# Kernel optimization log

Hardware: AMD Instinct MI355X
Metric: run time of the kernel (lower is better)

## Reference

```python
import jax, jax.numpy as jnp
import numpy as np
import math

DIM = 2048
NUM_HEADS = 16
NUM_KV_HEADS = 4
HEAD_DIM = DIM // NUM_HEADS  # 128
KV_DIM = DIM * NUM_KV_HEADS // NUM_HEADS  # 512
B, T = 4, 2048


def setup_inputs() -> dict:
    key = jax.random.key(0)
    ks = jax.random.split(key, 12)
    s = 0.02
    return {
        "x": jax.random.normal(ks[0], (B, T, DIM), dtype=jnp.float32),
        "cos": jax.random.uniform(ks[1], (T, HEAD_DIM // 2), dtype=jnp.float32),
        "sin": jax.random.uniform(ks[2], (T, HEAD_DIM // 2), dtype=jnp.float32),
        "Wq": jax.random.normal(ks[3], (DIM, DIM), dtype=jnp.float32) * s,
        "bq": jnp.zeros((DIM,), dtype=jnp.float32),
        "Wk": jax.random.normal(ks[4], (DIM, KV_DIM), dtype=jnp.float32) * s,
        "bk": jnp.zeros((KV_DIM,), dtype=jnp.float32),
        "Wv": jax.random.normal(ks[5], (DIM, KV_DIM), dtype=jnp.float32) * s,
        "bv": jnp.zeros((KV_DIM,), dtype=jnp.float32),
        "Wo": jax.random.normal(ks[6], (DIM, DIM), dtype=jnp.float32) * s,
        "bo": jnp.zeros((DIM,), dtype=jnp.float32),
    }


def _rope(t, cos, sin):
    # t: [B, H, T, D]; cos/sin: [T, D/2] broadcast over (B, H)
    t1, t2 = t[..., ::2], t[..., 1::2]
    return jnp.concatenate([t1 * cos - t2 * sin, t1 * sin + t2 * cos], axis=-1)


def reference(x, cos, sin, Wq, bq, Wk, bk, Wv, bv, Wo, bo):
    Bx, Tx, C = x.shape
    q = (x @ Wq + bq).reshape(Bx, Tx, NUM_HEADS, HEAD_DIM).transpose(0, 2, 1, 3)
    k = (x @ Wk + bk).reshape(Bx, Tx, NUM_KV_HEADS, HEAD_DIM).transpose(0, 2, 1, 3)
    v = (x @ Wv + bv).reshape(Bx, Tx, NUM_KV_HEADS, HEAD_DIM).transpose(0, 2, 1, 3)
    rep = NUM_HEADS // NUM_KV_HEADS
    k = jnp.repeat(k, rep, axis=1)
    v = jnp.repeat(v, rep, axis=1)
    q = _rope(q, cos, sin)
    k = _rope(k, cos, sin)
    scores = jnp.einsum("bhqd,bhkd->bhqk", q, k) / math.sqrt(HEAD_DIM)
    attn = jax.nn.softmax(scores, axis=-1)
    out = jnp.einsum("bhqk,bhkd->bhqd", attn, v)
    out = out.transpose(0, 2, 1, 3).reshape(Bx, Tx, C)
    return out @ Wo + bo
```

## Files before the change

### kernel.cpp

```cpp
#include <hip/hip_runtime.h>

typedef unsigned short u16;
using bf16x8 = __attribute__((ext_vector_type(8))) short;
using u16x8  = __attribute__((ext_vector_type(8))) unsigned short;
using f32x4  = __attribute__((ext_vector_type(4))) float;
using u32x2  = __attribute__((ext_vector_type(2))) unsigned int;

__device__ __forceinline__ u16 f2bf(float f) {
  unsigned u = __float_as_uint(f);
  u += 0x7FFFu + ((u >> 16) & 1u);
  return (u16)(u >> 16);
}

__device__ __forceinline__ unsigned cvt_pk_bf16(float lo, float hi) {
  unsigned r;
  asm("v_cvt_pk_bf16_f32 %0, %1, %2" : "=v"(r) : "v"(lo), "v"(hi));
  return r;
}

__device__ __forceinline__ void gload_lds16(const void* g, void* l) {
  __builtin_amdgcn_global_load_lds(
      (const __attribute__((address_space(1))) unsigned int*)g,
      (__attribute__((address_space(3))) unsigned int*)l, 16, 0, 0);
}

__global__ __launch_bounds__(256) void k_cvt(const float* __restrict__ src,
                                             u16* __restrict__ dst) {
  size_t i = (size_t)blockIdx.x * 256 + threadIdx.x;
  const float4* s4 = (const float4*)src;
  float4 a = s4[i * 2], b = s4[i * 2 + 1];
  u16x8 r;
  r[0] = f2bf(a.x); r[1] = f2bf(a.y); r[2] = f2bf(a.z); r[3] = f2bf(a.w);
  r[4] = f2bf(b.x); r[5] = f2bf(b.y); r[6] = f2bf(b.z); r[7] = f2bf(b.w);
  *(u16x8*)(dst + i * 8) = r;
}

__global__ void k_transpose_cvt(const float* __restrict__ src, u16* __restrict__ dst,
                                int R, int C) {
  __shared__ float tile[32][33];
  int bx = blockIdx.x * 32, by = blockIdx.y * 32;
  int tx = threadIdx.x, ty = threadIdx.y;
#pragma unroll
  for (int j = 0; j < 4; ++j)
    tile[ty + j * 8][tx] = src[(size_t)(by + ty + j * 8) * C + bx + tx];
  __syncthreads();
#pragma unroll
  for (int j = 0; j < 4; ++j)
    dst[(size_t)(bx + ty + j * 8) * R + by + tx] = f2bf(tile[tx][ty + j * 8]);
}

template <int EPI>
__global__ __launch_bounds__(512, 2) void k_gemm256(
    const u16* __restrict__ A, const u16* __restrict__ Bt,
    const float* __restrict__ bq, const float* __restrict__ bk, const float* __restrict__ bv,
    const float* __restrict__ cosb, const float* __restrict__ sinb,
    u16* __restrict__ qbuf, u16* __restrict__ kbuf, u16* __restrict__ vbufT,
    const float* __restrict__ bo, float* __restrict__ fout, int ntiles) {
  __shared__ u16 As[2][2][128 * 64];
  __shared__ u16 Bs[2][2][128 * 64];

  const int nwg = 32 * ntiles;
  const int per = nwg >> 3;
  const int sid = ((int)blockIdx.x & 7) * per + ((int)blockIdx.x >> 3);
  const int mt = sid & 31;
  const int nt = sid >> 5;

  const int tid = threadIdx.x, lane = tid & 63, w = tid >> 6;
  const int lm = lane & 15, lg = lane >> 4;
  const int wr = w >> 2, wc = w & 3;

  const u16* Abase = A  + (size_t)mt * 256 * 2048;
  const u16* Bbase = Bt + (size_t)nt * 256 * 2048;

  f32x4 acc[8][4];
#pragma unroll
  for (int mf = 0; mf < 8; ++mf)
#pragma unroll
    for (int nf = 0; nf < 4; ++nf) { f32x4 z = {0.f, 0.f, 0.f, 0.f}; acc[mf][nf] = z; }

  auto stage = [&](int d, int kt) {
#pragma unroll
    for (int j = 0; j < 2; ++j) {
      const int s = w * 2 + j;
      const int c = s * 64 + lane;
      const int row = c >> 3;
      const int col = ((c & 7) ^ (row & 7)) << 3;
#pragma unroll
      for (int h = 0; h < 2; ++h) {
        gload_lds16(Abase + (size_t)(h * 128 + row) * 2048 + kt + col, &As[d][h][s * 512]);
        gload_lds16(Bbase + (size_t)(h * 128 + row) * 2048 + kt + col, &Bs[d][h][s * 512]);
      }
    }
  };

  stage(0, 0);
  for (int t = 0; t < 32; ++t) {
    if (t < 31) {
      stage((t + 1) & 1, (t + 1) << 6);
      asm volatile("s_waitcnt vmcnt(8)" ::: "memory");
    } else {
      asm volatile("s_waitcnt vmcnt(0)" ::: "memory");
    }
    __builtin_amdgcn_s_barrier();
    __builtin_amdgcn_sched_barrier(0);

    const int d = t & 1;
    const u16* Ah = &As[d][wr][0];
    const u16* Bh = &Bs[d][wc >> 1][0];
    const int brow0 = (wc & 1) * 64;

    bf16x8 bfr[4][2];
#pragma unroll
    for (int nf = 0; nf < 4; ++nf)
#pragma unroll
      for (int k2 = 0; k2 < 2; ++k2) {
        const int row = brow0 + nf * 16 + lm;
        bfr[nf][k2] = *(const bf16x8*)(Bh + row * 64 + ((((k2 << 2) + lg) ^ (lm & 7)) << 3));
      }
#pragma unroll
    for (int mp = 0; mp < 4; ++mp) {
      bf16x8 af[2][2];
#pragma unroll
      for (int mi = 0; mi < 2; ++mi)
#pragma unroll
        for (int k2 = 0; k2 < 2; ++k2) {
          const int row = (mp * 2 + mi) * 16 + lm;
          af[mi][k2] = *(const bf16x8*)(Ah + row * 64 + ((((k2 << 2) + lg) ^ (lm & 7)) << 3));
        }
      __builtin_amdgcn_s_setprio(1);
#pragma unroll
      for (int mi = 0; mi < 2; ++mi)
#pragma unroll
        for (int k2 = 0; k2 < 2; ++k2)
#pragma unroll
          for (int nf = 0; nf < 4; ++nf)
            acc[mp * 2 + mi][nf] = __builtin_amdgcn_mfma_f32_16x16x32_bf16(
                af[mi][k2], bfr[nf][k2], acc[mp * 2 + mi][nf], 0, 0, 0);
      __builtin_amdgcn_s_setprio(0);
    }
    __builtin_amdgcn_sched_barrier(0);
    __builtin_amdgcn_s_barrier();
  }

  const int row0 = mt * 256 + wr * 128 + lg * 4;
  const int col0 = nt * 256 + wc * 64 + lm;
  const float qscale = 0.12751744f;

#pragma unroll
  for (int mf = 0; mf < 8; ++mf) {
#pragma unroll
    for (int nf = 0; nf < 4; ++nf) {
      const int gc = col0 + nf * 16;
#pragma unroll
      for (int i = 0; i < 4; ++i) {
        const int gr = row0 + mf * 16 + i;
        float v = acc[mf][nf][i];
        if (EPI == 1) {
          fout[(size_t)gr * 2048 + gc] = v + bo[gc];
        } else {
          const int b = gr >> 11, tt = gr & 2047;
          if (nt < 8) {
            const int h = gc >> 7, dd0 = gc & 127;
            float val = v + bq[gc];
            float part = __shfl_xor(val, 1);
            const int ir = dd0 >> 1;
            float c = cosb[tt * 64 + ir], s = sinb[tt * 64 + ir];
            float outv; int dd;
            if (dd0 & 1) { outv = part * s + val * c; dd = ir + 64; }
            else         { outv = val * c - part * s; dd = ir; }
            qbuf[(((size_t)(b * 16 + h) * 2048 + tt) << 7) + dd] = f2bf(outv * qscale);
          } else if (nt < 10) {
            const int g2 = gc - 2048;
            const int kvh = g2 >> 7, dd0 = g2 & 127;
            float val = v + bk[g2];
            float part = __shfl_xor(val, 1);
            const int ir = dd0 >> 1;
            float c = cosb[tt * 64 + ir], s = sinb[tt * 64 + ir];
            float outv; int dd;
            if (dd0 & 1) { outv = part * s + val * c; dd = ir + 64; }
            else         { outv = val * c - part * s; dd = ir; }
            kbuf[(((size_t)(b * 4 + kvh) * 2048 + tt) << 7) + dd] = f2bf(outv);
          } else {
            const int g2 = gc - 2560;
            const int kvh = g2 >> 7, dd0 = g2 & 127;
            float val = v + bv[g2];
            vbufT[((size_t)((b * 4 + kvh) * 128 + dd0)) * 2048 + tt] = f2bf(val);
          }
        }
      }
    }
  }
}

__global__ __launch_bounds__(256, 2) void k_attn(const u16* __restrict__ qbuf,
                                                 const u16* __restrict__ kbuf,
                                                 const u16* __restrict__ vbufT,
                                                 u16* __restrict__ ob) {
  __shared__ u16 Ks[2][64 * 128];
  __shared__ u16 Vs[2][128 * 64];
  __shared__ u16 Ps[128 * 64];

  const int f = blockIdx.x;
  const int x = f & 7, mm = f >> 3;
  const int g = x * 2 + (mm >> 6);
  const int mem = mm & 63;
  const int b = g >> 2, kvh = g & 3;
  const int h = kvh * 4 + (mem >> 4);
  const int qt = mem & 15;

  const int tid = threadIdx.x, lane = tid & 63, w = tid >> 6;
  const int lm = lane & 15, lg = lane >> 4;

  const u16* qb = qbuf + ((size_t)((b * 16 + h) * 2048 + qt * 128)) * 128;
  const u16* kb = kbuf + ((size_t)(b * 4 + kvh) * 2048) * 128;
  const u16* vb = vbufT + ((size_t)(b * 4 + kvh) * 128) * 2048;

  bf16x8 qf[2][4];
#pragma unroll
  for (int st = 0; st < 2; ++st)
#pragma unroll
    for (int dc = 0; dc < 4; ++dc)
      qf[st][dc] = *(const bf16x8*)(qb + (size_t)(w * 32 + st * 16 + lm) * 128 + dc * 32 + (lg << 3));

  f32x4 o[2][8];
#pragma unroll
  for (int st = 0; st < 2; ++st)
#pragma unroll
    for (int dn = 0; dn < 8; ++dn) { f32x4 z = {0.f, 0.f, 0.f, 0.f}; o[st][dn] = z; }
  float lsum[2] = {0.f, 0.f};

  auto stage = [&](int buf, int kt) {
#pragma unroll
    for (int j = 0; j < 4; ++j) {
      int s  = w * 4 + j;
      int cK = s * 64 + lane;
      int rK = cK >> 4, ccK = cK & 15;
      gload_lds16(kb + (size_t)(kt + rK) * 128 + ((ccK ^ (rK & 7)) << 3), &Ks[buf][s << 9]);
      int dV = s * 8 + (lane >> 3), ccV = lane & 7;
      gload_lds16(vb + (size_t)dV * 2048 + kt + ((ccV ^ (dV & 7)) << 3), &Vs[buf][s << 9]);
    }
  };

  stage(0, 0);
  int cur = 0;
  for (int t = 0; t < 32; ++t) {
    const int kt = t << 6;
    if (t < 31) {
      stage(cur ^ 1, kt + 64);
      asm volatile("s_waitcnt vmcnt(8)" ::: "memory");
    } else {
      asm volatile("s_waitcnt vmcnt(0)" ::: "memory");
    }
    __builtin_amdgcn_s_barrier();
    __builtin_amdgcn_sched_barrier(0);
    const u16* KsC = Ks[cur];
    const u16* VsC = Vs[cur];

#pragma unroll
    for (int kg = 0; kg < 4; ++kg) {
      const int krow = kg * 16 + lm;
      bf16x8 kf[4];
#pragma unroll
      for (int dc = 0; dc < 4; ++dc)
        kf[dc] = *(const bf16x8*)(KsC + krow * 128 + (((dc * 4 + lg) ^ (krow & 7)) << 3));
      f32x4 s0 = {0.f, 0.f, 0.f, 0.f}, s1 = {0.f, 0.f, 0.f, 0.f};
      __builtin_amdgcn_s_setprio(1);
#pragma unroll
      for (int dc = 0; dc < 4; ++dc) {
        s0 = __builtin_amdgcn_mfma_f32_16x16x32_bf16(kf[dc], qf[0][dc], s0, 0, 0, 0);
        s1 = __builtin_amdgcn_mfma_f32_16x16x32_bf16(kf[dc], qf[1][dc], s1, 0, 0, 0);
      }
      __builtin_amdgcn_s_setprio(0);
#pragma unroll
      for (int st = 0; st < 2; ++st) {
        f32x4 sv = st ? s1 : s0;
        float p0 = __builtin_amdgcn_exp2f(sv[0]);
        float p1 = __builtin_amdgcn_exp2f(sv[1]);
        float p2 = __builtin_amdgcn_exp2f(sv[2]);
        float p3 = __builtin_amdgcn_exp2f(sv[3]);
        lsum[st] += (p0 + p1) + (p2 + p3);
        u32x2 pk;
        pk[0] = cvt_pk_bf16(p0, p1);
        pk[1] = cvt_pk_bf16(p2, p3);
        const int q = w * 32 + st * 16 + lm;
        const int chunk = kg * 2 + (lg >> 1);
        u16* dst = Ps + q * 64 + ((chunk ^ (q & 7)) << 3) + ((lg & 1) << 2);
        *reinterpret_cast<u32x2*>(dst) = pk;
      }
    }

#pragma unroll
    for (int kstep = 0; kstep < 2; ++kstep) {
      bf16x8 pf[2];
#pragma unroll
      for (int st = 0; st < 2; ++st) {
        const int q = w * 32 + st * 16 + lm;
        pf[st] = *(const bf16x8*)(Ps + q * 64 + (((kstep * 4 + lg) ^ (q & 7)) << 3));
      }
      __builtin_amdgcn_s_setprio(1);
#pragma unroll
      for (int dn = 0; dn < 8; ++dn) {
        const int d = dn * 16 + lm;
        bf16x8 vf = *(const bf16x8*)(VsC + d * 64 + (((kstep * 4 + lg) ^ (d & 7)) << 3));
        o[0][dn] = __builtin_amdgcn_mfma_f32_16x16x32_bf16(pf[0], vf, o[0][dn], 0, 0, 0);
        o[1][dn] = __builtin_amdgcn_mfma_f32_16x16x32_bf16(pf[1], vf, o[1][dn], 0, 0, 0);
      }
      __builtin_amdgcn_s_setprio(0);
    }
    __builtin_amdgcn_sched_barrier(0);
    __builtin_amdgcn_s_barrier();
    cur ^= 1;
  }

#pragma unroll
  for (int st = 0; st < 2; ++st) {
    float L = lsum[st];
    L += __shfl_xor(L, 16);
    L += __shfl_xor(L, 32);
#pragma unroll
    for (int i = 0; i < 4; ++i) {
      float inv = 1.0f / __shfl(L, lg * 4 + i);
      int t = qt * 128 + w * 32 + st * 16 + lg * 4 + i;
#pragma unroll
      for (int dn = 0; dn < 8; ++dn) {
        int d = dn * 16 + lm;
        ob[((size_t)(b * 2048 + t)) * 2048 + h * 128 + d] = f2bf(o[st][dn][i] * inv);
      }
    }
  }
}

extern "C" void kernel_launch(void* const* d_in, const int* in_sizes, int n_in,
                              void* d_out, int out_size, void* d_ws, size_t ws_size,
                              hipStream_t stream) {
  const float* x    = (const float*)d_in[0];
  const float* cosb = (const float*)d_in[1];
  const float* sinb = (const float*)d_in[2];
  const float* Wq   = (const float*)d_in[3];
  const float* bq   = (const float*)d_in[4];
  const float* Wk   = (const float*)d_in[5];
  const float* bk   = (const float*)d_in[6];
  const float* Wv   = (const float*)d_in[7];
  const float* bv   = (const float*)d_in[8];
  const float* Wo   = (const float*)d_in[9];
  const float* bo   = (const float*)d_in[10];
  float* out = (float*)d_out;

  u16* ws    = (u16*)d_ws;
  u16* xb    = ws;
  u16* wqkvT = xb    + (size_t)8192 * 2048;
  u16* woT   = wqkvT + (size_t)3072 * 2048;
  u16* qbuf  = woT   + (size_t)2048 * 2048;
  u16* kbuf  = qbuf  + (size_t)8192 * 2048;
  u16* vbufT = kbuf  + (size_t)8192 * 512;
  u16* attn  = xb;

  k_cvt<<<8192, 256, 0, stream>>>(x, xb);
  dim3 tb(32, 8);
  k_transpose_cvt<<<dim3(64, 64), tb, 0, stream>>>(Wq, wqkvT, 2048, 2048);
  k_transpose_cvt<<<dim3(16, 64), tb, 0, stream>>>(Wk, wqkvT + (size_t)2048 * 2048, 2048, 512);
  k_transpose_cvt<<<dim3(16, 64), tb, 0, stream>>>(Wv, wqkvT + (size_t)2560 * 2048, 2048, 512);
  k_transpose_cvt<<<dim3(64, 64), tb, 0, stream>>>(Wo, woT, 2048, 2048);

  k_gemm256<0><<<384, 512, 0, stream>>>(xb, wqkvT, bq, bk, bv, cosb, sinb,
                                        qbuf, kbuf, vbufT, nullptr, nullptr, 12);
  k_attn<<<1024, 256, 0, stream>>>(qbuf, kbuf, vbufT, attn);
  k_gemm256<1><<<256, 512, 0, stream>>>(attn, woT, nullptr, nullptr, nullptr, nullptr, nullptr,
                                        nullptr, nullptr, nullptr, bo, out, 8);
}
```

Before: 444.1 us.

## Shrink GEMM tiles to 256x128 with BK=32 for higher occupancy

Both projection GEMMs move from 256x256 tiles with K-step 64 to 256x128 tiles with K-step 32. This cuts shared memory and accumulator registers per workgroup, so launch bounds can ask for 4 workgroups per CU and the grid doubles to 768 and 512 workgroups. The LDS swizzle and the wait counts are reworked to match. In exchange there are twice as many barrier-synchronised K iterations, and each workgroup does fewer MFMAs between loads, so data reuse drops.

```diff
diff --git a/kernel.cpp b/kernel.cpp
--- a/kernel.cpp
+++ b/kernel.cpp
@@ -50,16 +50,16 @@
 }
 
 template <int EPI>
-__global__ __launch_bounds__(512, 2) void k_gemm256(
+__global__ __launch_bounds__(512, 4) void k_gemm(
     const u16* __restrict__ A, const u16* __restrict__ Bt,
     const float* __restrict__ bq, const float* __restrict__ bk, const float* __restrict__ bv,
     const float* __restrict__ cosb, const float* __restrict__ sinb,
     u16* __restrict__ qbuf, u16* __restrict__ kbuf, u16* __restrict__ vbufT,
-    const float* __restrict__ bo, float* __restrict__ fout, int ntiles) {
-  __shared__ u16 As[2][2][128 * 64];
-  __shared__ u16 Bs[2][2][128 * 64];
-
-  const int nwg = 32 * ntiles;
+    const float* __restrict__ bo, float* __restrict__ fout, int ntn) {
+  __shared__ u16 As[2][256 * 32];
+  __shared__ u16 Bs[2][128 * 32];
+
+  const int nwg = 32 * ntn;
   const int per = nwg >> 3;
   const int sid = ((int)blockIdx.x & 7) * per + ((int)blockIdx.x >> 3);
   const int mt = sid & 31;
@@ -67,37 +67,37 @@
 
   const int tid = threadIdx.x, lane = tid & 63, w = tid >> 6;
   const int lm = lane & 15, lg = lane >> 4;
-  const int wr = w >> 2, wc = w & 3;
+  const int wr = w >> 1, wc = w & 1;
+  const int sw = (lm >> 1) & 3;
 
   const u16* Abase = A  + (size_t)mt * 256 * 2048;
-  const u16* Bbase = Bt + (size_t)nt * 256 * 2048;
-
-  f32x4 acc[8][4];
-#pragma unroll
-  for (int mf = 0; mf < 8; ++mf)
+  const u16* Bbase = Bt + (size_t)nt * 128 * 2048;
+
+  f32x4 acc[4][4];
+#pragma unroll
+  for (int mf = 0; mf < 4; ++mf)
 #pragma unroll
     for (int nf = 0; nf < 4; ++nf) { f32x4 z = {0.f, 0.f, 0.f, 0.f}; acc[mf][nf] = z; }
 
   auto stage = [&](int d, int kt) {
 #pragma unroll
     for (int j = 0; j < 2; ++j) {
-      const int s = w * 2 + j;
-      const int c = s * 64 + lane;
-      const int row = c >> 3;
-      const int col = ((c & 7) ^ (row & 7)) << 3;
-#pragma unroll
-      for (int h = 0; h < 2; ++h) {
-        gload_lds16(Abase + (size_t)(h * 128 + row) * 2048 + kt + col, &As[d][h][s * 512]);
-        gload_lds16(Bbase + (size_t)(h * 128 + row) * 2048 + kt + col, &Bs[d][h][s * 512]);
-      }
-    }
+      const int c = (w * 2 + j) * 64 + lane;
+      const int row = c >> 2;
+      const int cc = (c & 3) ^ ((row >> 1) & 3);
+      gload_lds16(Abase + (size_t)row * 2048 + kt + cc * 8, &As[d][(w * 2 + j) * 512]);
+    }
+    const int c = w * 64 + lane;
+    const int row = c >> 2;
+    const int cc = (c & 3) ^ ((row >> 1) & 3);
+    gload_lds16(Bbase + (size_t)row * 2048 + kt + cc * 8, &Bs[d][w * 512]);
   };
 
   stage(0, 0);
-  for (int t = 0; t < 32; ++t) {
-    if (t < 31) {
-      stage((t + 1) & 1, (t + 1) << 6);
-      asm volatile("s_waitcnt vmcnt(8)" ::: "memory");
+  for (int t = 0; t < 64; ++t) {
+    if (t < 63) {
+      stage((t + 1) & 1, (t + 1) << 5);
+      asm volatile("s_waitcnt vmcnt(3)" ::: "memory");
     } else {
       asm volatile("s_waitcnt vmcnt(0)" ::: "memory");
     }
@@ -105,49 +105,34 @@
     __builtin_amdgcn_sched_barrier(0);
 
     const int d = t & 1;
-    const u16* Ah = &As[d][wr][0];
-    const u16* Bh = &Bs[d][wc >> 1][0];
-    const int brow0 = (wc & 1) * 64;
-
-    bf16x8 bfr[4][2];
-#pragma unroll
-    for (int nf = 0; nf < 4; ++nf)
-#pragma unroll
-      for (int k2 = 0; k2 < 2; ++k2) {
-        const int row = brow0 + nf * 16 + lm;
-        bfr[nf][k2] = *(const bf16x8*)(Bh + row * 64 + ((((k2 << 2) + lg) ^ (lm & 7)) << 3));
-      }
-#pragma unroll
-    for (int mp = 0; mp < 4; ++mp) {
-      bf16x8 af[2][2];
-#pragma unroll
-      for (int mi = 0; mi < 2; ++mi)
-#pragma unroll
-        for (int k2 = 0; k2 < 2; ++k2) {
-          const int row = (mp * 2 + mi) * 16 + lm;
-          af[mi][k2] = *(const bf16x8*)(Ah + row * 64 + ((((k2 << 2) + lg) ^ (lm & 7)) << 3));
-        }
-      __builtin_amdgcn_s_setprio(1);
-#pragma unroll
-      for (int mi = 0; mi < 2; ++mi)
-#pragma unroll
-        for (int k2 = 0; k2 < 2; ++k2)
-#pragma unroll
-          for (int nf = 0; nf < 4; ++nf)
-            acc[mp * 2 + mi][nf] = __builtin_amdgcn_mfma_f32_16x16x32_bf16(
-                af[mi][k2], bfr[nf][k2], acc[mp * 2 + mi][nf], 0, 0, 0);
-      __builtin_amdgcn_s_setprio(0);
-    }
+    bf16x8 bfr[4], af[4];
+#pragma unroll
+    for (int nf = 0; nf < 4; ++nf) {
+      const int row = wc * 64 + nf * 16 + lm;
+      bfr[nf] = *(const bf16x8*)(&Bs[d][row * 32 + ((lg ^ sw) << 3)]);
+    }
+#pragma unroll
+    for (int mf = 0; mf < 4; ++mf) {
+      const int row = wr * 64 + mf * 16 + lm;
+      af[mf] = *(const bf16x8*)(&As[d][row * 32 + ((lg ^ sw) << 3)]);
+    }
+    __builtin_amdgcn_s_setprio(1);
+#pragma unroll
+    for (int mf = 0; mf < 4; ++mf)
+#pragma unroll
+      for (int nf = 0; nf < 4; ++nf)
+        acc[mf][nf] = __builtin_amdgcn_mfma_f32_16x16x32_bf16(af[mf], bfr[nf], acc[mf][nf], 0, 0, 0);
+    __builtin_amdgcn_s_setprio(0);
     __builtin_amdgcn_sched_barrier(0);
     __builtin_amdgcn_s_barrier();
   }
 
-  const int row0 = mt * 256 + wr * 128 + lg * 4;
-  const int col0 = nt * 256 + wc * 64 + lm;
+  const int row0 = mt * 256 + wr * 64 + lg * 4;
+  const int col0 = nt * 128 + wc * 64 + lm;
   const float qscale = 0.12751744f;
 
 #pragma unroll
-  for (int mf = 0; mf < 8; ++mf) {
+  for (int mf = 0; mf < 4; ++mf) {
 #pragma unroll
     for (int nf = 0; nf < 4; ++nf) {
       const int gc = col0 + nf * 16;
@@ -159,7 +144,7 @@
           fout[(size_t)gr * 2048 + gc] = v + bo[gc];
         } else {
           const int b = gr >> 11, tt = gr & 2047;
-          if (nt < 8) {
+          if (nt < 16) {
             const int h = gc >> 7, dd0 = gc & 127;
             float val = v + bq[gc];
             float part = __shfl_xor(val, 1);
@@ -169,7 +154,7 @@
             if (dd0 & 1) { outv = part * s + val * c; dd = ir + 64; }
             else         { outv = val * c - part * s; dd = ir; }
             qbuf[(((size_t)(b * 16 + h) * 2048 + tt) << 7) + dd] = f2bf(outv * qscale);
-          } else if (nt < 10) {
+          } else if (nt < 20) {
             const int g2 = gc - 2048;
             const int kvh = g2 >> 7, dd0 = g2 & 127;
             float val = v + bk[g2];
@@ -362,9 +347,9 @@
   k_transpose_cvt<<<dim3(16, 64), tb, 0, stream>>>(Wv, wqkvT + (size_t)2560 * 2048, 2048, 512);
   k_transpose_cvt<<<dim3(64, 64), tb, 0, stream>>>(Wo, woT, 2048, 2048);
 
-  k_gemm256<0><<<384, 512, 0, stream>>>(xb, wqkvT, bq, bk, bv, cosb, sinb,
-                                        qbuf, kbuf, vbufT, nullptr, nullptr, 12);
+  k_gemm<0><<<768, 512, 0, stream>>>(xb, wqkvT, bq, bk, bv, cosb, sinb,
+                                     qbuf, kbuf, vbufT, nullptr, nullptr, 24);
   k_attn<<<1024, 256, 0, stream>>>(qbuf, kbuf, vbufT, attn);
-  k_gemm256<1><<<256, 512, 0, stream>>>(attn, woT, nullptr, nullptr, nullptr, nullptr, nullptr,
-                                        nullptr, nullptr, nullptr, bo, out, 8);
-}
+  k_gemm<1><<<512, 512, 0, stream>>>(attn, woT, nullptr, nullptr, nullptr, nullptr, nullptr,
+                                     nullptr, nullptr, nullptr, bo, out, 16);
+}
```

After: 421.9 us. 5.0% less time.

## Restructure GEMM main loop into four-phase ping-pong with interleaved LDS reads

Applied to the files above, without the earlier changes.

Rewrites the 256x256 bf16 GEMM K-loop into four MFMA sub-phases (quadrants of the wave tile). LDS fragment loads for the next quadrant sit between them, and the next K-tile's global-to-LDS prefetch is issued early in the iteration. Barriers and setprio around each phase are meant to make co-resident waves alternate between memory and MFMA work, hiding load latency. LDS staging becomes a flat 256-row buffer. The cost is more barriers per iteration and a full vmcnt(0) wait before the last phase.

```diff
diff --git a/kernel.cpp b/kernel.cpp
--- a/kernel.cpp
+++ b/kernel.cpp
@@ -50,24 +50,25 @@
 }
 
 template <int EPI>
-__global__ __launch_bounds__(512, 2) void k_gemm256(
+__global__ __launch_bounds__(512, 2) void k_gemm256p(
     const u16* __restrict__ A, const u16* __restrict__ Bt,
     const float* __restrict__ bq, const float* __restrict__ bk, const float* __restrict__ bv,
     const float* __restrict__ cosb, const float* __restrict__ sinb,
     u16* __restrict__ qbuf, u16* __restrict__ kbuf, u16* __restrict__ vbufT,
-    const float* __restrict__ bo, float* __restrict__ fout, int ntiles) {
-  __shared__ u16 As[2][2][128 * 64];
-  __shared__ u16 Bs[2][2][128 * 64];
-
-  const int nwg = 32 * ntiles;
+    const float* __restrict__ bo, float* __restrict__ fout, int nnt) {
+  __shared__ u16 As[2][256 * 64];
+  __shared__ u16 Bs[2][256 * 64];
+
+  const int nwg = 32 * nnt;
   const int per = nwg >> 3;
   const int sid = ((int)blockIdx.x & 7) * per + ((int)blockIdx.x >> 3);
-  const int mt = sid & 31;
-  const int nt = sid >> 5;
+  const int mt = sid % 32;
+  const int nt = sid / 32;
 
   const int tid = threadIdx.x, lane = tid & 63, w = tid >> 6;
   const int lm = lane & 15, lg = lane >> 4;
   const int wr = w >> 2, wc = w & 3;
+  const int sw = lm & 7;
 
   const u16* Abase = A  + (size_t)mt * 256 * 2048;
   const u16* Bbase = Bt + (size_t)nt * 256 * 2048;
@@ -78,68 +79,114 @@
 #pragma unroll
     for (int nf = 0; nf < 4; ++nf) { f32x4 z = {0.f, 0.f, 0.f, 0.f}; acc[mf][nf] = z; }
 
-  auto stage = [&](int d, int kt) {
-#pragma unroll
-    for (int j = 0; j < 2; ++j) {
-      const int s = w * 2 + j;
-      const int c = s * 64 + lane;
-      const int row = c >> 3;
-      const int col = ((c & 7) ^ (row & 7)) << 3;
-#pragma unroll
-      for (int h = 0; h < 2; ++h) {
-        gload_lds16(Abase + (size_t)(h * 128 + row) * 2048 + kt + col, &As[d][h][s * 512]);
-        gload_lds16(Bbase + (size_t)(h * 128 + row) * 2048 + kt + col, &Bs[d][h][s * 512]);
-      }
+  auto stage4 = [&](u16* dst, const u16* src, int kt) {
+#pragma unroll
+    for (int gI = 0; gI < 4; ++gI) {
+      const int c = gI * 512 + tid;
+      const int row = c >> 3, cc = c & 7;
+      gload_lds16(src + (size_t)row * 2048 + kt + ((cc ^ (row & 7)) << 3),
+                  dst + ((gI * 512 + (w << 6)) << 3));
     }
   };
 
-  stage(0, 0);
+  const int arow = wr * 128 + lm;
+  const int brow = wc * 64 + lm;
+
+  stage4(As[0], Abase, 0);
+  stage4(Bs[0], Bbase, 0);
+  asm volatile("s_waitcnt vmcnt(0)" ::: "memory");
+  __builtin_amdgcn_s_barrier();
+
   for (int t = 0; t < 32; ++t) {
+    const int d = t & 1;
+    const u16* Ab = As[d];
+    const u16* Bb = Bs[d];
+    bf16x8 a03[8], b01[4], b23[4], a47[8];
+
+#pragma unroll
+    for (int mf = 0; mf < 4; ++mf)
+#pragma unroll
+      for (int kh = 0; kh < 2; ++kh) {
+        const int row = arow + mf * 16;
+        a03[mf * 2 + kh] = *(const bf16x8*)(Ab + (((row << 3) + (((kh << 2) + lg) ^ sw)) << 3));
+      }
+#pragma unroll
+    for (int nf = 0; nf < 2; ++nf)
+#pragma unroll
+      for (int kh = 0; kh < 2; ++kh) {
+        const int row = brow + nf * 16;
+        b01[nf * 2 + kh] = *(const bf16x8*)(Bb + (((row << 3) + (((kh << 2) + lg) ^ sw)) << 3));
+      }
     if (t < 31) {
-      stage((t + 1) & 1, (t + 1) << 6);
-      asm volatile("s_waitcnt vmcnt(8)" ::: "memory");
-    } else {
-      asm volatile("s_waitcnt vmcnt(0)" ::: "memory");
-    }
-    __builtin_amdgcn_s_barrier();
-    __builtin_amdgcn_sched_barrier(0);
-
-    const int d = t & 1;
-    const u16* Ah = &As[d][wr][0];
-    const u16* Bh = &Bs[d][wc >> 1][0];
-    const int brow0 = (wc & 1) * 64;
-
-    bf16x8 bfr[4][2];
-#pragma unroll
-    for (int nf = 0; nf < 4; ++nf)
-#pragma unroll
-      for (int k2 = 0; k2 < 2; ++k2) {
-        const int row = brow0 + nf * 16 + lm;
-        bfr[nf][k2] = *(const bf16x8*)(Bh + row * 64 + ((((k2 << 2) + lg) ^ (lm & 7)) << 3));
-      }
-#pragma unroll
-    for (int mp = 0; mp < 4; ++mp) {
-      bf16x8 af[2][2];
-#pragma unroll
-      for (int mi = 0; mi < 2; ++mi)
-#pragma unroll
-        for (int k2 = 0; k2 < 2; ++k2) {
-          const int row = (mp * 2 + mi) * 16 + lm;
-          af[mi][k2] = *(const bf16x8*)(Ah + row * 64 + ((((k2 << 2) + lg) ^ (lm & 7)) << 3));
-        }
-      __builtin_amdgcn_s_setprio(1);
-#pragma unroll
-      for (int mi = 0; mi < 2; ++mi)
-#pragma unroll
-        for (int k2 = 0; k2 < 2; ++k2)
-#pragma unroll
-          for (int nf = 0; nf < 4; ++nf)
-            acc[mp * 2 + mi][nf] = __builtin_amdgcn_mfma_f32_16x16x32_bf16(
-                af[mi][k2], bfr[nf][k2], acc[mp * 2 + mi][nf], 0, 0, 0);
-      __builtin_amdgcn_s_setprio(0);
-    }
-    __builtin_amdgcn_sched_barrier(0);
-    __builtin_amdgcn_s_barrier();
+      stage4(As[d ^ 1], Abase, (t + 1) << 6);
+      stage4(Bs[d ^ 1], Bbase, (t + 1) << 6);
+    }
+    __builtin_amdgcn_s_barrier();
+    __builtin_amdgcn_s_setprio(1);
+#pragma unroll
+    for (int mf = 0; mf < 4; ++mf)
+#pragma unroll
+      for (int nf = 0; nf < 2; ++nf)
+#pragma unroll
+        for (int kh = 0; kh < 2; ++kh)
+          acc[mf][nf] = __builtin_amdgcn_mfma_f32_16x16x32_bf16(
+              a03[mf * 2 + kh], b01[nf * 2 + kh], acc[mf][nf], 0, 0, 0);
+    __builtin_amdgcn_s_setprio(0);
+    __builtin_amdgcn_s_barrier();
+
+#pragma unroll
+    for (int nf = 0; nf < 2; ++nf)
+#pragma unroll
+      for (int kh = 0; kh < 2; ++kh) {
+        const int row = brow + (nf + 2) * 16;
+        b23[nf * 2 + kh] = *(const bf16x8*)(Bb + (((row << 3) + (((kh << 2) + lg) ^ sw)) << 3));
+      }
+    __builtin_amdgcn_s_barrier();
+    __builtin_amdgcn_s_setprio(1);
+#pragma unroll
+    for (int mf = 0; mf < 4; ++mf)
+#pragma unroll
+      for (int nf = 0; nf < 2; ++nf)
+#pragma unroll
+        for (int kh = 0; kh < 2; ++kh)
+          acc[mf][nf + 2] = __builtin_amdgcn_mfma_f32_16x16x32_bf16(
+              a03[mf * 2 + kh], b23[nf * 2 + kh], acc[mf][nf + 2], 0, 0, 0);
+    __builtin_amdgcn_s_setprio(0);
+    __builtin_amdgcn_s_barrier();
+
+#pragma unroll
+    for (int mf = 0; mf < 4; ++mf)
+#pragma unroll
+      for (int kh = 0; kh < 2; ++kh) {
+        const int row = arow + (mf + 4) * 16;
+        a47[mf * 2 + kh] = *(const bf16x8*)(Ab + (((row << 3) + (((kh << 2) + lg) ^ sw)) << 3));
+      }
+    __builtin_amdgcn_s_barrier();
+    __builtin_amdgcn_s_setprio(1);
+#pragma unroll
+    for (int mf = 0; mf < 4; ++mf)
+#pragma unroll
+      for (int nf = 0; nf < 2; ++nf)
+#pragma unroll
+        for (int kh = 0; kh < 2; ++kh)
+          acc[mf + 4][nf + 2] = __builtin_amdgcn_mfma_f32_16x16x32_bf16(
+              a47[mf * 2 + kh], b23[nf * 2 + kh], acc[mf + 4][nf + 2], 0, 0, 0);
+    __builtin_amdgcn_s_setprio(0);
+    __builtin_amdgcn_s_barrier();
+
+    asm volatile("s_waitcnt vmcnt(0)" ::: "memory");
+    __builtin_amdgcn_s_barrier();
+    __builtin_amdgcn_s_setprio(1);
+#pragma unroll
+    for (int mf = 0; mf < 4; ++mf)
+#pragma unroll
+      for (int nf = 0; nf < 2; ++nf)
+#pragma unroll
+        for (int kh = 0; kh < 2; ++kh)
+          acc[mf + 4][nf] = __builtin_amdgcn_mfma_f32_16x16x32_bf16(
+              a47[mf * 2 + kh], b01[nf * 2 + kh], acc[mf + 4][nf], 0, 0, 0);
+    __builtin_amdgcn_s_setprio(0);
+    __syncthreads();
   }
 
   const int row0 = mt * 256 + wr * 128 + lg * 4;
@@ -362,9 +409,9 @@
   k_transpose_cvt<<<dim3(16, 64), tb, 0, stream>>>(Wv, wqkvT + (size_t)2560 * 2048, 2048, 512);
   k_transpose_cvt<<<dim3(64, 64), tb, 0, stream>>>(Wo, woT, 2048, 2048);
 
-  k_gemm256<0><<<384, 512, 0, stream>>>(xb, wqkvT, bq, bk, bv, cosb, sinb,
-                                        qbuf, kbuf, vbufT, nullptr, nullptr, 12);
+  k_gemm256p<0><<<384, 512, 0, stream>>>(xb, wqkvT, bq, bk, bv, cosb, sinb,
+                                         qbuf, kbuf, vbufT, nullptr, nullptr, 12);
   k_attn<<<1024, 256, 0, stream>>>(qbuf, kbuf, vbufT, attn);
-  k_gemm256<1><<<256, 512, 0, stream>>>(attn, woT, nullptr, nullptr, nullptr, nullptr, nullptr,
-                                        nullptr, nullptr, nullptr, bo, out, 8);
-}
+  k_gemm256p<1><<<256, 512, 0, stream>>>(attn, woT, nullptr, nullptr, nullptr, nullptr, nullptr,
+                                         nullptr, nullptr, nullptr, bo, out, 8);
+}
```

Result: slower. 461.3 us (+3.9%).
